# Performance work log

Hardware: AMD Instinct MI355X
Metric: run time of the kernel (lower is better)

## Reference

```python
import jax, jax.numpy as jnp
import numpy as np

INPUT_DIM = 24
HIDDEN = 128
NUM_LAYERS = 3
OUTPUT_DIM = 1


def _lstm_layer(x, Wih, Whh, bih, bhh):
    """Single LSTM layer, PyTorch gate order (i, f, g, o). x: [B,T,D] -> [B,T,H]."""
    B = x.shape[0]
    H = Whh.shape[1]
    # Precompute input projections for all timesteps at once: [B,T,4H]
    xg = jnp.einsum('btd,gd->btg', x, Wih) + bih
    xg = jnp.swapaxes(xg, 0, 1)  # [T,B,4H]
    h0 = jnp.zeros((B, H), x.dtype)
    c0 = jnp.zeros((B, H), x.dtype)

    def step(carry, xt):
        h, c = carry
        gates = xt + h @ Whh.T + bhh  # [B,4H]
        i, f, g, o = jnp.split(gates, 4, axis=-1)
        i = jax.nn.sigmoid(i)
        f = jax.nn.sigmoid(f)
        g = jnp.tanh(g)
        o = jax.nn.sigmoid(o)
        c = f * c + i * g
        h = o * jnp.tanh(c)
        return (h, c), h

    _, hs = jax.lax.scan(step, (h0, c0), xg)  # hs: [T,B,H]
    return jnp.swapaxes(hs, 0, 1)  # [B,T,H]


def setup_inputs() -> dict:
    key = jax.random.key(0)
    ks = jax.random.split(key, 16)
    B, T = 2048, 256
    s = 0.05
    inp = {
        'x': jax.random.normal(ks[0], (B, T, INPUT_DIM), dtype=jnp.float32),
    }
    dims_in = [INPUT_DIM, HIDDEN, HIDDEN]
    for l in range(NUM_LAYERS):
        inp[f'Wih{l}'] = jax.random.normal(ks[1 + 4 * l], (4 * HIDDEN, dims_in[l]), dtype=jnp.float32) * s
        inp[f'Whh{l}'] = jax.random.normal(ks[2 + 4 * l], (4 * HIDDEN, HIDDEN), dtype=jnp.float32) * s
        inp[f'bih{l}'] = jax.random.normal(ks[3 + 4 * l], (4 * HIDDEN,), dtype=jnp.float32) * s
        inp[f'bhh{l}'] = jax.random.normal(ks[4 + 4 * l], (4 * HIDDEN,), dtype=jnp.float32) * s
    inp['Wfc'] = jax.random.normal(ks[13], (OUTPUT_DIM, HIDDEN), dtype=jnp.float32) * s
    inp['bfc'] = jax.random.normal(ks[14], (OUTPUT_DIM,), dtype=jnp.float32) * s
    return inp


def reference(x, Wih0, Whh0, bih0, bhh0, Wih1, Whh1, bih1, bhh1,
              Wih2, Whh2, bih2, bhh2, Wfc, bfc):
    # 3 stacked LSTM layers (dropout inactive in eval mode), zero initial state.
    h = _lstm_layer(x, Wih0, Whh0, bih0, bhh0)
    h = _lstm_layer(h, Wih1, Whh1, bih1, bhh1)
    h = _lstm_layer(h, Wih2, Whh2, bih2, bhh2)
    # Linear projection of the final timestep: [B,1]
    return h[:, -1, :] @ Wfc.T + bfc
```

## Files before the change

### kernel.cpp

```cpp
#include <hip/hip_runtime.h>

#define T_STEPS 256
#define BATCH   2048
#define HID     128
#define BH      (BATCH * HID)

typedef short short8  __attribute__((ext_vector_type(8)));
typedef float float4v __attribute__((ext_vector_type(4)));

__device__ __forceinline__ unsigned short f2bf(float f) {
    unsigned int u = __builtin_bit_cast(unsigned int, f);
    u += 0x7fffu + ((u >> 16) & 1u);
    return (unsigned short)(u >> 16);
}
__device__ __forceinline__ float bf2f(unsigned short b) {
    unsigned int u = ((unsigned int)b) << 16;
    return __builtin_bit_cast(float, u);
}

#if __has_builtin(__builtin_amdgcn_exp2f)
#define EXP2F(x) __builtin_amdgcn_exp2f(x)
#else
#define EXP2F(x) exp2f(x)
#endif
__device__ __forceinline__ float sigf(float x) {
    return __builtin_amdgcn_rcpf(1.0f + EXP2F(x * -1.442695041f));
}
__device__ __forceinline__ float tanh_fast(float x) {
    return 2.0f * __builtin_amdgcn_rcpf(1.0f + EXP2F(x * -2.885390082f)) - 1.0f;
}

__device__ __forceinline__ void block_sync_lds() {
    asm volatile("s_waitcnt lgkmcnt(0)" ::: "memory");
    __builtin_amdgcn_s_barrier();
    __builtin_amdgcn_sched_barrier(0);
}

__device__ __forceinline__ int lposH(int row, int off) {
    return row * 256 + (off ^ ((row & 7) << 4));
}
__device__ __forceinline__ int lposX(int row, int off) {
    return row * 256 + (off ^ ((row & 7) << 4));
}
__device__ __forceinline__ int lposX0(int row, int off) {
    return row * 64 + (off ^ ((row & 3) << 4));
}
__device__ __forceinline__ int lposG(int q, int row, int col) {
    return (q * 8 + row) * 512 + ((col * 4) ^ ((row & 2) << 5));
}

__device__ __forceinline__ short8 load_w8(const float* __restrict__ p) {
    float4v a = *reinterpret_cast<const float4v*>(p);
    float4v b = *reinterpret_cast<const float4v*>(p + 4);
    short8 r;
    r[0] = (short)f2bf(a[0]); r[1] = (short)f2bf(a[1]);
    r[2] = (short)f2bf(a[2]); r[3] = (short)f2bf(a[3]);
    r[4] = (short)f2bf(b[0]); r[5] = (short)f2bf(b[1]);
    r[6] = (short)f2bf(b[2]); r[7] = (short)f2bf(b[3]);
    return r;
}

#define LDS_BYTES 77824

template<bool IS_L0, bool WRITE_H, bool FINAL>
__device__ __forceinline__ void lstm_phase(
    unsigned char* a_lds,
    const float* __restrict__ x0,
    const float* __restrict__ Wih,
    const float* __restrict__ Whh,
    const float* __restrict__ bih,
    const float* __restrict__ bhh,
    unsigned short* __restrict__ hbuf,
    const float* __restrict__ Wfc,
    const float* __restrict__ bfc,
    float* __restrict__ out,
    const int tid, const int b0)
{
    constexpr int XKS = IS_L0 ? 1 : 4;
    constexpr int XRB = IS_L0 ? 64 : 256;
    constexpr int HB  = 2048;
    constexpr int XB  = 16 * XRB;
    constexpr int SL0 = 2 * HB;
    constexpr int SL1 = 2 * HB + XB;
    constexpr int XGB = 2 * HB + 2 * XB;
    constexpr int PARS  = 16384;
    constexpr int PAIRS = 32768;

    const int lane  = tid & 63;
    const int wv    = tid >> 6;
    const int t16   = lane & 15;
    const int kgrp8 = (lane >> 4) * 8;
    const bool upper = lane >= 32;
    const int row0  = ((lane >> 4) & 1) * 4 + ((lane >> 5) & 1) * 2;

    {
        short8 z = {0,0,0,0,0,0,0,0};
        for (int a = tid * 16; a < 2 * HB + 2 * XB; a += 512 * 16)
            *reinterpret_cast<short8*>(&a_lds[a]) = z;
    }
    __syncthreads();

    if (tid < 256) {
        const int jA = 32 * wv + t16, jB = jA + 16;
        const int g2 = t16 >> 2;
        const int hrow = ((g2 & 1) << 2) | ((g2 >> 1) << 1) | (t16 & 1);
        int aoffH[4];
        #pragma unroll
        for (int ks = 0; ks < 4; ++ks)
            aoffH[ks] = lposH(hrow, ks * 64 + kgrp8 * 2);
        int hst[2][2];
        hst[0][0] = lposH(row0,     2 * jA);
        hst[0][1] = lposH(row0 + 1, 2 * jA);
        hst[1][0] = lposH(row0,     2 * jB);
        hst[1][1] = lposH(row0 + 1, 2 * jB);
        int xgr[2][4];
        #pragma unroll
        for (int c = 0; c < 2; ++c)
            #pragma unroll
            for (int q = 0; q < 4; ++q)
                xgr[c][q] = XGB + lposG(q, row0, c ? jB : jA);

        short8 wfh[2][4][4];
        #pragma unroll
        for (int c = 0; c < 2; ++c)
            #pragma unroll
            for (int q = 0; q < 4; ++q) {
                const int n = 128 * q + (c ? jB : jA);
                #pragma unroll
                for (int ks = 0; ks < 4; ++ks)
                    wfh[c][q][ks] = load_w8(Whh + n * 128 + ks * 32 + kgrp8);
            }

        float crA0 = 0.f, crA1 = 0.f, crB0 = 0.f, crB1 = 0.f;
        block_sync_lds();
        block_sync_lds();

        auto hstep = [&](const int rb, const int wb, const int xgo) {
            short8 hva[4];
            #pragma unroll
            for (int ks = 0; ks < 4; ++ks)
                hva[ks] = *reinterpret_cast<const short8*>(&a_lds[rb + aoffH[ks]]);
            float4v acc[2][4];
            #pragma unroll
            for (int c = 0; c < 2; ++c)
                #pragma unroll
                for (int q = 0; q < 4; ++q) {
                    const float v0 = *reinterpret_cast<const float*>(&a_lds[xgo + xgr[c][q]]);
                    const float v1 = *reinterpret_cast<const float*>(&a_lds[xgo + xgr[c][q] + 512]);
                    acc[c][q] = float4v{v0, v1, v0, v1};
                }
            __builtin_amdgcn_s_setprio(1);
            #pragma unroll
            for (int ks = 0; ks < 4; ++ks)
                #pragma unroll
                for (int c = 0; c < 2; ++c)
                    #pragma unroll
                    for (int q = 0; q < 4; ++q)
                        acc[c][q] = __builtin_amdgcn_mfma_f32_16x16x32_bf16(
                            hva[ks], wfh[c][q][ks], acc[c][q], 0, 0, 0);
            __builtin_amdgcn_s_setprio(0);
            {
                const float i0 = upper ? acc[0][0][2] : acc[0][0][0];
                const float i1 = upper ? acc[0][0][3] : acc[0][0][1];
                const float f0 = upper ? acc[0][1][2] : acc[0][1][0];
                const float f1 = upper ? acc[0][1][3] : acc[0][1][1];
                const float g0 = upper ? acc[0][2][2] : acc[0][2][0];
                const float g1 = upper ? acc[0][2][3] : acc[0][2][1];
                const float o0 = upper ? acc[0][3][2] : acc[0][3][0];
                const float o1 = upper ? acc[0][3][3] : acc[0][3][1];
                const float c0 = sigf(f0) * crA0 + sigf(i0) * tanh_fast(g0);
                const float c1 = sigf(f1) * crA1 + sigf(i1) * tanh_fast(g1);
                crA0 = c0;  crA1 = c1;
                const float h0 = sigf(o0) * tanh_fast(c0);
                const float h1 = sigf(o1) * tanh_fast(c1);
                unsigned int pk;
                asm("v_cvt_pk_bf16_f32 %0, %1, %2" : "=v"(pk) : "v"(h0), "v"(h1));
                *reinterpret_cast<unsigned short*>(&a_lds[wb + hst[0][0]]) =
                    (unsigned short)(pk & 0xffffu);
                *reinterpret_cast<unsigned short*>(&a_lds[wb + hst[0][1]]) =
                    (unsigned short)(pk >> 16);
            }
            {
                const float i0 = upper ? acc[1][0][2] : acc[1][0][0];
                const float i1 = upper ? acc[1][0][3] : acc[1][0][1];
                const float f0 = upper ? acc[1][1][2] : acc[1][1][0];
                const float f1 = upper ? acc[1][1][3] : acc[1][1][1];
                const float g0 = upper ? acc[1][2][2] : acc[1][2][0];
                const float g1 = upper ? acc[1][2][3] : acc[1][2][1];
                const float o0 = upper ? acc[1][3][2] : acc[1][3][0];
                const float o1 = upper ? acc[1][3][3] : acc[1][3][1];
                const float c0 = sigf(f0) * crB0 + sigf(i0) * tanh_fast(g0);
                const float c1 = sigf(f1) * crB1 + sigf(i1) * tanh_fast(g1);
                crB0 = c0;  crB1 = c1;
                const float h0 = sigf(o0) * tanh_fast(c0);
                const float h1 = sigf(o1) * tanh_fast(c1);
                unsigned int pk;
                asm("v_cvt_pk_bf16_f32 %0, %1, %2" : "=v"(pk) : "v"(h0), "v"(h1));
                *reinterpret_cast<unsigned short*>(&a_lds[wb + hst[1][0]]) =
                    (unsigned short)(pk & 0xffffu);
                *reinterpret_cast<unsigned short*>(&a_lds[wb + hst[1][1]]) =
                    (unsigned short)(pk >> 16);
            }
            block_sync_lds();
        };

        for (int mm = 0; mm < T_STEPS / 4; ++mm) {
            hstep(0,  HB, 0);
            hstep(HB, 0,  PARS);
            hstep(0,  HB, PAIRS);
            hstep(HB, 0,  PAIRS + PARS);
        }
    } else {
        const int jA = 32 * (wv - 4) + t16, jB = jA + 16;
        const int tid2 = tid & 255;
        const int sh_row = tid2 >> 5, sh_c8 = tid2 & 31;
        const int hroff8 = lposH(sh_row, sh_c8 * 8);
        const size_t sgoff8 = (size_t)(b0 + sh_row) * HID + sh_c8 * 4;
        const int sar = tid2 >> 4, sc16 = tid2 & 15;
        const int sb  = (sar & 1) | (((sar >> 3) & 1) << 1) | (((sar >> 2) & 1) << 2);
        const int ss  = (sar >> 1) & 1;
        const int xwoff = lposX(sar, sc16 * 16);
        const size_t xgrow = (size_t)(b0 + sb) * HID + sc16 * 8;
        const bool xvalid = sc16 < 12;
        const int xw0off = lposX0(sar, sc16 * 4);
        const size_t x0row = (size_t)(b0 + sb) * (T_STEPS * 24) + sc16 * 2;
        int aoffX[XKS];
        #pragma unroll
        for (int s = 0; s < XKS; ++s)
            aoffX[s] = IS_L0 ? lposX0(t16, kgrp8 * 2)
                             : lposX(t16, s * 64 + kgrp8 * 2);
        int xgw[2][4];
        #pragma unroll
        for (int c = 0; c < 2; ++c)
            #pragma unroll
            for (int q = 0; q < 4; ++q)
                xgw[c][q] = XGB + lposG(q, row0, c ? jB : jA);

        short8 wfx[2][4][XKS];
        float  bias[2][4];
        #pragma unroll
        for (int c = 0; c < 2; ++c)
            #pragma unroll
            for (int q = 0; q < 4; ++q) {
                const int n = 128 * q + (c ? jB : jA);
                bias[c][q] = bih[n] + bhh[n];
                if constexpr (IS_L0) {
                    if (kgrp8 < 24) wfx[c][q][0] = load_w8(Wih + n * 24 + kgrp8);
                    else { short8 z = {0,0,0,0,0,0,0,0}; wfx[c][q][0] = z; }
                } else {
                    #pragma unroll
                    for (int s = 0; s < 4; ++s)
                        wfx[c][q][s] = load_w8(Wih + n * 128 + s * 32 + kgrp8);
                }
            }

        if constexpr (!IS_L0) {
            short8 v0 = *reinterpret_cast<const short8*>(&hbuf[(size_t)(0 + ss) * BH + xgrow]);
            short8 v1 = *reinterpret_cast<const short8*>(&hbuf[(size_t)(2 + ss) * BH + xgrow]);
            *reinterpret_cast<short8*>(&a_lds[SL0 + xwoff]) = v0;
            *reinterpret_cast<short8*>(&a_lds[SL1 + xwoff]) = v1;
        } else if (xvalid) {
            float2 a = *reinterpret_cast<const float2*>(&x0[x0row + (size_t)(0 + ss) * 24]);
            float2 b = *reinterpret_cast<const float2*>(&x0[x0row + (size_t)(2 + ss) * 24]);
            unsigned int pa, pb;
            asm("v_cvt_pk_bf16_f32 %0, %1, %2" : "=v"(pa) : "v"(a.x), "v"(a.y));
            asm("v_cvt_pk_bf16_f32 %0, %1, %2" : "=v"(pb) : "v"(b.x), "v"(b.y));
            *reinterpret_cast<unsigned int*>(&a_lds[SL0 + xw0off]) = pa;
            *reinterpret_cast<unsigned int*>(&a_lds[SL1 + xw0off]) = pb;
        }
        block_sync_lds();

        float4v xacc[2][4];
        auto xinit = [&]() {
            #pragma unroll
            for (int c = 0; c < 2; ++c)
                #pragma unroll
                for (int q = 0; q < 4; ++q)
                    xacc[c][q] = float4v{bias[c][q], bias[c][q], bias[c][q], bias[c][q]};
        };
        auto xmfma2 = [&](const int SLrd, const int s0) {
            short8 a0 = *reinterpret_cast<const short8*>(&a_lds[SLrd + aoffX[s0]]);
            short8 a1 = *reinterpret_cast<const short8*>(&a_lds[SLrd + aoffX[s0 + 1]]);
            #pragma unroll
            for (int c = 0; c < 2; ++c)
                #pragma unroll
                for (int q = 0; q < 4; ++q)
                    xacc[c][q] = __builtin_amdgcn_mfma_f32_16x16x32_bf16(
                        a0, wfx[c][q][s0], xacc[c][q], 0, 0, 0);
            #pragma unroll
            for (int c = 0; c < 2; ++c)
                #pragma unroll
                for (int q = 0; q < 4; ++q)
                    xacc[c][q] = __builtin_amdgcn_mfma_f32_16x16x32_bf16(
                        a1, wfx[c][q][s0 + 1], xacc[c][q], 0, 0, 0);
        };
        auto xmfma1 = [&](const int SLrd) {
            short8 a0 = *reinterpret_cast<const short8*>(&a_lds[SLrd + aoffX[0]]);
            #pragma unroll
            for (int c = 0; c < 2; ++c)
                #pragma unroll
                for (int q = 0; q < 4; ++q)
                    xacc[c][q] = __builtin_amdgcn_mfma_f32_16x16x32_bf16(
                        a0, wfx[c][q][0], xacc[c][q], 0, 0, 0);
        };
        auto xgwrite = [&](const int XGP) {
            #pragma unroll
            for (int c = 0; c < 2; ++c)
                #pragma unroll
                for (int q = 0; q < 4; ++q) {
                    *reinterpret_cast<float*>(&a_lds[XGP + xgw[c][q]])              = xacc[c][q][0];
                    *reinterpret_cast<float*>(&a_lds[XGP + xgw[c][q] + 512])        = xacc[c][q][1];
                    *reinterpret_cast<float*>(&a_lds[XGP + PARS + xgw[c][q]])       = xacc[c][q][2];
                    *reinterpret_cast<float*>(&a_lds[XGP + PARS + xgw[c][q] + 512]) = xacc[c][q][3];
                }
        };

        xinit();
        if constexpr (!IS_L0) { xmfma2(SL0, 0); xmfma2(SL0, 2); }
        else xmfma1(SL0);
        xgwrite(0);
        block_sync_lds();

        short8 xpre = {0,0,0,0,0,0,0,0};
        float2 xpf  = {0.f, 0.f};

        auto xstepE = [&](int t, const int SLrd) {
            if (WRITE_H && t > 0) {
                int2 hv = *reinterpret_cast<const int2*>(&a_lds[0 + hroff8]);
                *reinterpret_cast<int2*>(&hbuf[(size_t)(t - 1) * BH + sgoff8]) = hv;
            }
            int tl = t + 4 + ss;  tl = tl < T_STEPS ? tl : T_STEPS - 1;
            if constexpr (!IS_L0)
                xpre = *reinterpret_cast<const short8*>(&hbuf[(size_t)tl * BH + xgrow]);
            else if (xvalid)
                xpf = *reinterpret_cast<const float2*>(&x0[x0row + (size_t)tl * 24]);
            xinit();
            if constexpr (!IS_L0) xmfma2(SLrd, 0);
            else xmfma1(SLrd);
            block_sync_lds();
        };
        auto xstepO = [&](int t, const int SLrd, const int SLwr, const int XGP) {
            if (WRITE_H) {
                int2 hv = *reinterpret_cast<const int2*>(&a_lds[HB + hroff8]);
                *reinterpret_cast<int2*>(&hbuf[(size_t)(t - 1) * BH + sgoff8]) = hv;
            }
            if constexpr (!IS_L0)
                *reinterpret_cast<short8*>(&a_lds[SLwr + xwoff]) = xpre;
            else if (xvalid) {
                unsigned int p;
                asm("v_cvt_pk_bf16_f32 %0, %1, %2" : "=v"(p) : "v"(xpf.x), "v"(xpf.y));
                *reinterpret_cast<unsigned int*>(&a_lds[SLwr + xw0off]) = p;
            }
            if constexpr (!IS_L0) xmfma2(SLrd, 2);
            xgwrite(XGP);
            block_sync_lds();
        };

        for (int mm = 0; mm < T_STEPS / 4; ++mm) {
            const int t0 = 4 * mm;
            xstepE(t0,     SL1);
            xstepO(t0 + 1, SL1, SL0, PAIRS);
            xstepE(t0 + 2, SL0);
            xstepO(t0 + 3, SL0, SL1, 0);
        }
        if (WRITE_H) {
            int2 hv = *reinterpret_cast<const int2*>(&a_lds[0 + hroff8]);
            *reinterpret_cast<int2*>(&hbuf[(size_t)(T_STEPS - 1) * BH + sgoff8]) = hv;
        }
    }

    if (FINAL && tid < 128) {
        const int r = tid >> 4, seg = tid & 15;
        float s = 0.f;
        #pragma unroll
        for (int k = 0; k < 8; ++k) {
            const int j = seg * 8 + k;
            s += bf2f(*reinterpret_cast<const unsigned short*>(&a_lds[lposH(r, 2 * j)]))
                 * Wfc[j];
        }
        #pragma unroll
        for (int off = 8; off >= 1; off >>= 1) s += __shfl_xor(s, off);
        if (seg == 0) out[b0 + r] = s + bfc[0];
    }
}

__global__ __launch_bounds__(512, 2)
void lstm3(const float* __restrict__ x0,
           const float* __restrict__ Wih0, const float* __restrict__ Whh0,
           const float* __restrict__ bih0, const float* __restrict__ bhh0,
           const float* __restrict__ Wih1, const float* __restrict__ Whh1,
           const float* __restrict__ bih1, const float* __restrict__ bhh1,
           const float* __restrict__ Wih2, const float* __restrict__ Whh2,
           const float* __restrict__ bih2, const float* __restrict__ bhh2,
           const float* __restrict__ Wfc,  const float* __restrict__ bfc,
           unsigned short* __restrict__ hbuf, float* __restrict__ out)
{
    __shared__ __attribute__((aligned(16))) unsigned char a_lds[LDS_BYTES];
    const int tid = threadIdx.x;
    const int b0  = blockIdx.x * 8;

    lstm_phase<true,  true,  false>(a_lds, x0, Wih0, Whh0, bih0, bhh0, hbuf,
                                    nullptr, nullptr, nullptr, tid, b0);
    __syncthreads();
    lstm_phase<false, true,  false>(a_lds, nullptr, Wih1, Whh1, bih1, bhh1, hbuf,
                                    nullptr, nullptr, nullptr, tid, b0);
    __syncthreads();
    lstm_phase<false, false, true >(a_lds, nullptr, Wih2, Whh2, bih2, bhh2, hbuf,
                                    Wfc, bfc, out, tid, b0);
}

extern "C" void kernel_launch(void* const* d_in, const int* in_sizes, int n_in,
                              void* d_out, int out_size, void* d_ws, size_t ws_size,
                              hipStream_t stream) {
    (void)in_sizes; (void)n_in; (void)out_size; (void)ws_size;
    const float* x    = (const float*)d_in[0];
    const float* Wih0 = (const float*)d_in[1];
    const float* Whh0 = (const float*)d_in[2];
    const float* bih0 = (const float*)d_in[3];
    const float* bhh0 = (const float*)d_in[4];
    const float* Wih1 = (const float*)d_in[5];
    const float* Whh1 = (const float*)d_in[6];
    const float* bih1 = (const float*)d_in[7];
    const float* bhh1 = (const float*)d_in[8];
    const float* Wih2 = (const float*)d_in[9];
    const float* Whh2 = (const float*)d_in[10];
    const float* bih2 = (const float*)d_in[11];
    const float* bhh2 = (const float*)d_in[12];
    const float* Wfc  = (const float*)d_in[13];
    const float* bfc  = (const float*)d_in[14];
    float* out = (float*)d_out;
    unsigned short* hbuf = (unsigned short*)d_ws;

    dim3 grid(BATCH / 8), block(512);
    lstm3<<<grid, block, 0, stream>>>(x, Wih0, Whh0, bih0, bhh0,
                                      Wih1, Whh1, bih1, bhh1,
                                      Wih2, Whh2, bih2, bhh2,
                                      Wfc, bfc, hbuf, out);
}
```

Baseline: 637.8 us.

## Double block to 1024 threads, one 16-column tile per wave

The block grows from 512 to 1024 threads. Each of the eight recurrent waves and each of the eight input-projection waves now owns a single 16-column slice instead of two, which halves per-wave MFMA chains and gate math on the serial critical path. Staging loads and stores shrink to 4-element vectors so they cover the same data across more threads. The catch is that launch_bounds(1024,4) asks for tighter register limits, and four waves per SIMD with 1024-thread blocks raises occupancy and register pressure, which could spill the register-held weight fragments.

Result: faster. 562.0 us (-11.9%).

```diff
diff --git a/kernel.cpp b/kernel.cpp
--- a/kernel.cpp
+++ b/kernel.cpp
@@ -6,6 +6,7 @@
 #define BH      (BATCH * HID)
 
 typedef short short8  __attribute__((ext_vector_type(8)));
+typedef short short4v __attribute__((ext_vector_type(4)));
 typedef float float4v __attribute__((ext_vector_type(4)));
 
 __device__ __forceinline__ unsigned short f2bf(float f) {
@@ -90,48 +91,40 @@
     const int wv    = tid >> 6;
     const int t16   = lane & 15;
     const int kgrp8 = (lane >> 4) * 8;
-    const bool upper = lane >= 32;
     const int row0  = ((lane >> 4) & 1) * 4 + ((lane >> 5) & 1) * 2;
 
     {
         short8 z = {0,0,0,0,0,0,0,0};
-        for (int a = tid * 16; a < 2 * HB + 2 * XB; a += 512 * 16)
+        for (int a = tid * 16; a < 2 * HB + 2 * XB; a += 1024 * 16)
             *reinterpret_cast<short8*>(&a_lds[a]) = z;
     }
     __syncthreads();
 
-    if (tid < 256) {
-        const int jA = 32 * wv + t16, jB = jA + 16;
+    if (tid < 512) {
+        const int jcol = 16 * wv + t16;
         const int g2 = t16 >> 2;
         const int hrow = ((g2 & 1) << 2) | ((g2 >> 1) << 1) | (t16 & 1);
         int aoffH[4];
         #pragma unroll
         for (int ks = 0; ks < 4; ++ks)
             aoffH[ks] = lposH(hrow, ks * 64 + kgrp8 * 2);
-        int hst[2][2];
-        hst[0][0] = lposH(row0,     2 * jA);
-        hst[0][1] = lposH(row0 + 1, 2 * jA);
-        hst[1][0] = lposH(row0,     2 * jB);
-        hst[1][1] = lposH(row0 + 1, 2 * jB);
-        int xgr[2][4];
-        #pragma unroll
-        for (int c = 0; c < 2; ++c)
-            #pragma unroll
-            for (int q = 0; q < 4; ++q)
-                xgr[c][q] = XGB + lposG(q, row0, c ? jB : jA);
-
-        short8 wfh[2][4][4];
-        #pragma unroll
-        for (int c = 0; c < 2; ++c)
-            #pragma unroll
-            for (int q = 0; q < 4; ++q) {
-                const int n = 128 * q + (c ? jB : jA);
-                #pragma unroll
-                for (int ks = 0; ks < 4; ++ks)
-                    wfh[c][q][ks] = load_w8(Whh + n * 128 + ks * 32 + kgrp8);
-            }
-
-        float crA0 = 0.f, crA1 = 0.f, crB0 = 0.f, crB1 = 0.f;
+        const int hwoff0 = lposH(row0,     2 * jcol);
+        const int hwoff1 = lposH(row0 + 1, 2 * jcol);
+        int xgr[4];
+        #pragma unroll
+        for (int q = 0; q < 4; ++q)
+            xgr[q] = XGB + lposG(q, row0, jcol);
+
+        short8 wfh[4][4];
+        #pragma unroll
+        for (int q = 0; q < 4; ++q) {
+            const int n = 128 * q + jcol;
+            #pragma unroll
+            for (int ks = 0; ks < 4; ++ks)
+                wfh[q][ks] = load_w8(Whh + n * 128 + ks * 32 + kgrp8);
+        }
+
+        float cr0 = 0.f, cr1 = 0.f;
         block_sync_lds();
         block_sync_lds();
 
@@ -140,67 +133,32 @@
             #pragma unroll
             for (int ks = 0; ks < 4; ++ks)
                 hva[ks] = *reinterpret_cast<const short8*>(&a_lds[rb + aoffH[ks]]);
-            float4v acc[2][4];
-            #pragma unroll
-            for (int c = 0; c < 2; ++c)
-                #pragma unroll
-                for (int q = 0; q < 4; ++q) {
-                    const float v0 = *reinterpret_cast<const float*>(&a_lds[xgo + xgr[c][q]]);
-                    const float v1 = *reinterpret_cast<const float*>(&a_lds[xgo + xgr[c][q] + 512]);
-                    acc[c][q] = float4v{v0, v1, v0, v1};
-                }
+            float4v acc[4];
+            #pragma unroll
+            for (int q = 0; q < 4; ++q) {
+                const float v0 = *reinterpret_cast<const float*>(&a_lds[xgo + xgr[q]]);
+                const float v1 = *reinterpret_cast<const float*>(&a_lds[xgo + xgr[q] + 512]);
+                acc[q] = float4v{v0, v1, v0, v1};
+            }
             __builtin_amdgcn_s_setprio(1);
             #pragma unroll
             for (int ks = 0; ks < 4; ++ks)
                 #pragma unroll
-                for (int c = 0; c < 2; ++c)
-                    #pragma unroll
-                    for (int q = 0; q < 4; ++q)
-                        acc[c][q] = __builtin_amdgcn_mfma_f32_16x16x32_bf16(
-                            hva[ks], wfh[c][q][ks], acc[c][q], 0, 0, 0);
+                for (int q = 0; q < 4; ++q)
+                    acc[q] = __builtin_amdgcn_mfma_f32_16x16x32_bf16(
+                        hva[ks], wfh[q][ks], acc[q], 0, 0, 0);
             __builtin_amdgcn_s_setprio(0);
-            {
-                const float i0 = upper ? acc[0][0][2] : acc[0][0][0];
-                const float i1 = upper ? acc[0][0][3] : acc[0][0][1];
-                const float f0 = upper ? acc[0][1][2] : acc[0][1][0];
-                const float f1 = upper ? acc[0][1][3] : acc[0][1][1];
-                const float g0 = upper ? acc[0][2][2] : acc[0][2][0];
-                const float g1 = upper ? acc[0][2][3] : acc[0][2][1];
-                const float o0 = upper ? acc[0][3][2] : acc[0][3][0];
-                const float o1 = upper ? acc[0][3][3] : acc[0][3][1];
-                const float c0 = sigf(f0) * crA0 + sigf(i0) * tanh_fast(g0);
-                const float c1 = sigf(f1) * crA1 + sigf(i1) * tanh_fast(g1);
-                crA0 = c0;  crA1 = c1;
-                const float h0 = sigf(o0) * tanh_fast(c0);
-                const float h1 = sigf(o1) * tanh_fast(c1);
-                unsigned int pk;
-                asm("v_cvt_pk_bf16_f32 %0, %1, %2" : "=v"(pk) : "v"(h0), "v"(h1));
-                *reinterpret_cast<unsigned short*>(&a_lds[wb + hst[0][0]]) =
-                    (unsigned short)(pk & 0xffffu);
-                *reinterpret_cast<unsigned short*>(&a_lds[wb + hst[0][1]]) =
-                    (unsigned short)(pk >> 16);
-            }
-            {
-                const float i0 = upper ? acc[1][0][2] : acc[1][0][0];
-                const float i1 = upper ? acc[1][0][3] : acc[1][0][1];
-                const float f0 = upper ? acc[1][1][2] : acc[1][1][0];
-                const float f1 = upper ? acc[1][1][3] : acc[1][1][1];
-                const float g0 = upper ? acc[1][2][2] : acc[1][2][0];
-                const float g1 = upper ? acc[1][2][3] : acc[1][2][1];
-                const float o0 = upper ? acc[1][3][2] : acc[1][3][0];
-                const float o1 = upper ? acc[1][3][3] : acc[1][3][1];
-                const float c0 = sigf(f0) * crB0 + sigf(i0) * tanh_fast(g0);
-                const float c1 = sigf(f1) * crB1 + sigf(i1) * tanh_fast(g1);
-                crB0 = c0;  crB1 = c1;
-                const float h0 = sigf(o0) * tanh_fast(c0);
-                const float h1 = sigf(o1) * tanh_fast(c1);
-                unsigned int pk;
-                asm("v_cvt_pk_bf16_f32 %0, %1, %2" : "=v"(pk) : "v"(h0), "v"(h1));
-                *reinterpret_cast<unsigned short*>(&a_lds[wb + hst[1][0]]) =
-                    (unsigned short)(pk & 0xffffu);
-                *reinterpret_cast<unsigned short*>(&a_lds[wb + hst[1][1]]) =
-                    (unsigned short)(pk >> 16);
-            }
+            const float c0 = sigf(acc[1][0]) * cr0 + sigf(acc[0][0]) * tanh_fast(acc[2][0]);
+            const float c1 = sigf(acc[1][1]) * cr1 + sigf(acc[0][1]) * tanh_fast(acc[2][1]);
+            cr0 = c0;  cr1 = c1;
+            const float h0 = sigf(acc[3][0]) * tanh_fast(c0);
+            const float h1 = sigf(acc[3][1]) * tanh_fast(c1);
+            unsigned int pk;
+            asm("v_cvt_pk_bf16_f32 %0, %1, %2" : "=v"(pk) : "v"(h0), "v"(h1));
+            *reinterpret_cast<unsigned short*>(&a_lds[wb + hwoff0]) =
+                (unsigned short)(pk & 0xffffu);
+            *reinterpret_cast<unsigned short*>(&a_lds[wb + hwoff1]) =
+                (unsigned short)(pk >> 16);
             block_sync_lds();
         };
 
@@ -211,57 +169,60 @@
             hstep(HB, 0,  PAIRS + PARS);
         }
     } else {
-        const int jA = 32 * (wv - 4) + t16, jB = jA + 16;
-        const int tid2 = tid & 255;
-        const int sh_row = tid2 >> 5, sh_c8 = tid2 & 31;
-        const int hroff8 = lposH(sh_row, sh_c8 * 8);
-        const size_t sgoff8 = (size_t)(b0 + sh_row) * HID + sh_c8 * 4;
-        const int sar = tid2 >> 4, sc16 = tid2 & 15;
+        const int wx = wv - 8;
+        const int jX = 16 * wx + t16;
+        const int tid2 = tid - 512;
+        const int sh_row = tid2 >> 6, sh_c = tid2 & 63;
+        const int hroff4 = lposH(sh_row, sh_c * 4);
+        const size_t sgoff4 = (size_t)(b0 + sh_row) * HID + sh_c * 2;
+        const int sar = tid2 >> 5, sc8 = tid2 & 31;
         const int sb  = (sar & 1) | (((sar >> 3) & 1) << 1) | (((sar >> 2) & 1) << 2);
         const int ss  = (sar >> 1) & 1;
-        const int xwoff = lposX(sar, sc16 * 16);
-        const size_t xgrow = (size_t)(b0 + sb) * HID + sc16 * 8;
-        const bool xvalid = sc16 < 12;
-        const int xw0off = lposX0(sar, sc16 * 4);
-        const size_t x0row = (size_t)(b0 + sb) * (T_STEPS * 24) + sc16 * 2;
+        const int xwoff = lposX(sar, sc8 * 8);
+        const size_t xgrow = (size_t)(b0 + sb) * HID + sc8 * 4;
+        const int  tidL = tid2 & 255;
+        const bool l0act = tid2 < 256;
+        const int  sarL = tidL >> 4, sc16 = tidL & 15;
+        const int  sbL = (sarL & 1) | (((sarL >> 3) & 1) << 1) | (((sarL >> 2) & 1) << 2);
+        const int  ssL = (sarL >> 1) & 1;
+        const bool xvalid = l0act && (sc16 < 12);
+        const int  xw0off = lposX0(sarL, sc16 * 4);
+        const size_t x0row = (size_t)(b0 + sbL) * (T_STEPS * 24) + sc16 * 2;
+
         int aoffX[XKS];
         #pragma unroll
         for (int s = 0; s < XKS; ++s)
             aoffX[s] = IS_L0 ? lposX0(t16, kgrp8 * 2)
                              : lposX(t16, s * 64 + kgrp8 * 2);
-        int xgw[2][4];
-        #pragma unroll
-        for (int c = 0; c < 2; ++c)
-            #pragma unroll
-            for (int q = 0; q < 4; ++q)
-                xgw[c][q] = XGB + lposG(q, row0, c ? jB : jA);
-
-        short8 wfx[2][4][XKS];
-        float  bias[2][4];
-        #pragma unroll
-        for (int c = 0; c < 2; ++c)
-            #pragma unroll
-            for (int q = 0; q < 4; ++q) {
-                const int n = 128 * q + (c ? jB : jA);
-                bias[c][q] = bih[n] + bhh[n];
-                if constexpr (IS_L0) {
-                    if (kgrp8 < 24) wfx[c][q][0] = load_w8(Wih + n * 24 + kgrp8);
-                    else { short8 z = {0,0,0,0,0,0,0,0}; wfx[c][q][0] = z; }
-                } else {
-                    #pragma unroll
-                    for (int s = 0; s < 4; ++s)
-                        wfx[c][q][s] = load_w8(Wih + n * 128 + s * 32 + kgrp8);
-                }
-            }
+        int xgw[4];
+        #pragma unroll
+        for (int q = 0; q < 4; ++q)
+            xgw[q] = XGB + lposG(q, row0, jX);
+
+        short8 wfx[4][XKS];
+        float  bias[4];
+        #pragma unroll
+        for (int q = 0; q < 4; ++q) {
+            const int n = 128 * q + jX;
+            bias[q] = bih[n] + bhh[n];
+            if constexpr (IS_L0) {
+                if (kgrp8 < 24) wfx[q][0] = load_w8(Wih + n * 24 + kgrp8);
+                else { short8 z = {0,0,0,0,0,0,0,0}; wfx[q][0] = z; }
+            } else {
+                #pragma unroll
+                for (int s = 0; s < 4; ++s)
+                    wfx[q][s] = load_w8(Wih + n * 128 + s * 32 + kgrp8);
+            }
+        }
 
         if constexpr (!IS_L0) {
-            short8 v0 = *reinterpret_cast<const short8*>(&hbuf[(size_t)(0 + ss) * BH + xgrow]);
-            short8 v1 = *reinterpret_cast<const short8*>(&hbuf[(size_t)(2 + ss) * BH + xgrow]);
-            *reinterpret_cast<short8*>(&a_lds[SL0 + xwoff]) = v0;
-            *reinterpret_cast<short8*>(&a_lds[SL1 + xwoff]) = v1;
+            short4v v0 = *reinterpret_cast<const short4v*>(&hbuf[(size_t)(0 + ss) * BH + xgrow]);
+            short4v v1 = *reinterpret_cast<const short4v*>(&hbuf[(size_t)(2 + ss) * BH + xgrow]);
+            *reinterpret_cast<short4v*>(&a_lds[SL0 + xwoff]) = v0;
+            *reinterpret_cast<short4v*>(&a_lds[SL1 + xwoff]) = v1;
         } else if (xvalid) {
-            float2 a = *reinterpret_cast<const float2*>(&x0[x0row + (size_t)(0 + ss) * 24]);
-            float2 b = *reinterpret_cast<const float2*>(&x0[x0row + (size_t)(2 + ss) * 24]);
+            float2 a = *reinterpret_cast<const float2*>(&x0[x0row + (size_t)(0 + ssL) * 24]);
+            float2 b = *reinterpret_cast<const float2*>(&x0[x0row + (size_t)(2 + ssL) * 24]);
             unsigned int pa, pb;
             asm("v_cvt_pk_bf16_f32 %0, %1, %2" : "=v"(pa) : "v"(a.x), "v"(a.y));
             asm("v_cvt_pk_bf16_f32 %0, %1, %2" : "=v"(pb) : "v"(b.x), "v"(b.y));
@@ -270,49 +231,39 @@
         }
         block_sync_lds();
 
-        float4v xacc[2][4];
+        float4v xacc[4];
         auto xinit = [&]() {
             #pragma unroll
-            for (int c = 0; c < 2; ++c)
-                #pragma unroll
-                for (int q = 0; q < 4; ++q)
-                    xacc[c][q] = float4v{bias[c][q], bias[c][q], bias[c][q], bias[c][q]};
+            for (int q = 0; q < 4; ++q)
+                xacc[q] = float4v{bias[q], bias[q], bias[q], bias[q]};
         };
         auto xmfma2 = [&](const int SLrd, const int s0) {
             short8 a0 = *reinterpret_cast<const short8*>(&a_lds[SLrd + aoffX[s0]]);
             short8 a1 = *reinterpret_cast<const short8*>(&a_lds[SLrd + aoffX[s0 + 1]]);
             #pragma unroll
-            for (int c = 0; c < 2; ++c)
-                #pragma unroll
-                for (int q = 0; q < 4; ++q)
-                    xacc[c][q] = __builtin_amdgcn_mfma_f32_16x16x32_bf16(
-                        a0, wfx[c][q][s0], xacc[c][q], 0, 0, 0);
-            #pragma unroll
-            for (int c = 0; c < 2; ++c)
-                #pragma unroll
-                for (int q = 0; q < 4; ++q)
-                    xacc[c][q] = __builtin_amdgcn_mfma_f32_16x16x32_bf16(
-                        a1, wfx[c][q][s0 + 1], xacc[c][q], 0, 0, 0);
+            for (int q = 0; q < 4; ++q)
+                xacc[q] = __builtin_amdgcn_mfma_f32_16x16x32_bf16(
+                    a0, wfx[q][s0], xacc[q], 0, 0, 0);
+            #pragma unroll
+            for (int q = 0; q < 4; ++q)
+                xacc[q] = __builtin_amdgcn_mfma_f32_16x16x32_bf16(
+                    a1, wfx[q][s0 + 1], xacc[q], 0, 0, 0);
         };
         auto xmfma1 = [&](const int SLrd) {
             short8 a0 = *reinterpret_cast<const short8*>(&a_lds[SLrd + aoffX[0]]);
             #pragma unroll
-            for (int c = 0; c < 2; ++c)
-                #pragma unroll
-                for (int q = 0; q < 4; ++q)
-                    xacc[c][q] = __builtin_amdgcn_mfma_f32_16x16x32_bf16(
-                        a0, wfx[c][q][0], xacc[c][q], 0, 0, 0);
+            for (int q = 0; q < 4; ++q)
+                xacc[q] = __builtin_amdgcn_mfma_f32_16x16x32_bf16(
+                    a0, wfx[q][0], xacc[q], 0, 0, 0);
         };
         auto xgwrite = [&](const int XGP) {
             #pragma unroll
-            for (int c = 0; c < 2; ++c)
-                #pragma unroll
-                for (int q = 0; q < 4; ++q) {
-                    *reinterpret_cast<float*>(&a_lds[XGP + xgw[c][q]])              = xacc[c][q][0];
-                    *reinterpret_cast<float*>(&a_lds[XGP + xgw[c][q] + 512])        = xacc[c][q][1];
-                    *reinterpret_cast<float*>(&a_lds[XGP + PARS + xgw[c][q]])       = xacc[c][q][2];
-                    *reinterpret_cast<float*>(&a_lds[XGP + PARS + xgw[c][q] + 512]) = xacc[c][q][3];
-                }
+            for (int q = 0; q < 4; ++q) {
+                *reinterpret_cast<float*>(&a_lds[XGP + xgw[q]])              = xacc[q][0];
+                *reinterpret_cast<float*>(&a_lds[XGP + xgw[q] + 512])        = xacc[q][1];
+                *reinterpret_cast<float*>(&a_lds[XGP + PARS + xgw[q]])       = xacc[q][2];
+                *reinterpret_cast<float*>(&a_lds[XGP + PARS + xgw[q] + 512]) = xacc[q][3];
+            }
         };
 
         xinit();
@@ -321,19 +272,21 @@
         xgwrite(0);
         block_sync_lds();
 
-        short8 xpre = {0,0,0,0,0,0,0,0};
-        float2 xpf  = {0.f, 0.f};
+        short4v xpre = {0, 0, 0, 0};
+        float2  xpf  = {0.f, 0.f};
 
         auto xstepE = [&](int t, const int SLrd) {
             if (WRITE_H && t > 0) {
-                int2 hv = *reinterpret_cast<const int2*>(&a_lds[0 + hroff8]);
-                *reinterpret_cast<int2*>(&hbuf[(size_t)(t - 1) * BH + sgoff8]) = hv;
-            }
-            int tl = t + 4 + ss;  tl = tl < T_STEPS ? tl : T_STEPS - 1;
-            if constexpr (!IS_L0)
-                xpre = *reinterpret_cast<const short8*>(&hbuf[(size_t)tl * BH + xgrow]);
-            else if (xvalid)
+                unsigned int hv = *reinterpret_cast<const unsigned int*>(&a_lds[0 + hroff4]);
+                *reinterpret_cast<unsigned int*>(&hbuf[(size_t)(t - 1) * BH + sgoff4]) = hv;
+            }
+            if constexpr (!IS_L0) {
+                int tl = t + 4 + ss;  tl = tl < T_STEPS ? tl : T_STEPS - 1;
+                xpre = *reinterpret_cast<const short4v*>(&hbuf[(size_t)tl * BH + xgrow]);
+            } else if (xvalid) {
+                int tl = t + 4 + ssL;  tl = tl < T_STEPS ? tl : T_STEPS - 1;
                 xpf = *reinterpret_cast<const float2*>(&x0[x0row + (size_t)tl * 24]);
+            }
             xinit();
             if constexpr (!IS_L0) xmfma2(SLrd, 0);
             else xmfma1(SLrd);
@@ -341,11 +294,11 @@
         };
         auto xstepO = [&](int t, const int SLrd, const int SLwr, const int XGP) {
             if (WRITE_H) {
-                int2 hv = *reinterpret_cast<const int2*>(&a_lds[HB + hroff8]);
-                *reinterpret_cast<int2*>(&hbuf[(size_t)(t - 1) * BH + sgoff8]) = hv;
+                unsigned int hv = *reinterpret_cast<const unsigned int*>(&a_lds[HB + hroff4]);
+                *reinterpret_cast<unsigned int*>(&hbuf[(size_t)(t - 1) * BH + sgoff4]) = hv;
             }
             if constexpr (!IS_L0)
-                *reinterpret_cast<short8*>(&a_lds[SLwr + xwoff]) = xpre;
+                *reinterpret_cast<short4v*>(&a_lds[SLwr + xwoff]) = xpre;
             else if (xvalid) {
                 unsigned int p;
                 asm("v_cvt_pk_bf16_f32 %0, %1, %2" : "=v"(p) : "v"(xpf.x), "v"(xpf.y));
@@ -364,8 +317,8 @@
             xstepO(t0 + 3, SL0, SL1, 0);
         }
         if (WRITE_H) {
-            int2 hv = *reinterpret_cast<const int2*>(&a_lds[0 + hroff8]);
-            *reinterpret_cast<int2*>(&hbuf[(size_t)(T_STEPS - 1) * BH + sgoff8]) = hv;
+            unsigned int hv = *reinterpret_cast<const unsigned int*>(&a_lds[0 + hroff4]);
+            *reinterpret_cast<unsigned int*>(&hbuf[(size_t)(T_STEPS - 1) * BH + sgoff4]) = hv;
         }
     }
 
@@ -384,7 +337,7 @@
     }
 }
 
-__global__ __launch_bounds__(512, 2)
+__global__ __launch_bounds__(1024, 4)
 void lstm3(const float* __restrict__ x0,
            const float* __restrict__ Wih0, const float* __restrict__ Whh0,
            const float* __restrict__ bih0, const float* __restrict__ bhh0,
@@ -431,7 +384,7 @@
     float* out = (float*)d_out;
     unsigned short* hbuf = (unsigned short*)d_ws;
 
-    dim3 grid(BATCH / 8), block(512);
+    dim3 grid(BATCH / 8), block(1024);
     lstm3<<<grid, block, 0, stream>>>(x, Wih0, Whh0, bih0, bhh0,
                                       Wih1, Whh1, bih1, bhh1,
                                       Wih2, Whh2, bih2, bhh2,
```
